# Performance work log

Hardware: AMD Instinct MI355X
Metric: run time of the kernel (lower is better)

The kernel has to match this reference:

```python
import jax, jax.numpy as jnp
import numpy as np

TOTAL_WORDS = 10000
EMB = 100
SEQ = 80
UNITS = 64
BATCH = 8192


def setup_inputs() -> dict:
    key = jax.random.key(0)
    ks = jax.random.split(key, 10)
    sc = 0.05
    return {
        "tokens": jax.random.randint(ks[0], (BATCH, SEQ), 0, TOTAL_WORDS, dtype=jnp.int32),
        "emb": jax.random.normal(ks[1], (TOTAL_WORDS, EMB), jnp.float32) * sc,
        "W1x": jax.random.normal(ks[2], (EMB, UNITS), jnp.float32) * sc,
        "W1h": jax.random.normal(ks[3], (UNITS, UNITS), jnp.float32) * sc,
        "b1": jnp.zeros((UNITS,), jnp.float32),
        "W2x": jax.random.normal(ks[4], (UNITS, UNITS), jnp.float32) * sc,
        "W2h": jax.random.normal(ks[5], (UNITS, UNITS), jnp.float32) * sc,
        "b2": jnp.zeros((UNITS,), jnp.float32),
        "Wd": jax.random.normal(ks[6], (UNITS, 1), jnp.float32) * sc,
        "bd": jnp.zeros((1,), jnp.float32),
    }


def _simple_rnn(x, Wx, Wh, b):
    # x: [B, T, D] -> all hidden states [B, T, H] (Keras SimpleRNN, tanh)
    B = x.shape[0]
    H = Wh.shape[0]
    h0 = jnp.zeros((B, H), x.dtype)

    def step(h, xt):
        h = jnp.tanh(xt @ Wx + h @ Wh + b)
        return h, h

    _, hs = jax.lax.scan(step, h0, jnp.swapaxes(x, 0, 1))  # hs: [T, B, H]
    return jnp.swapaxes(hs, 0, 1)


def reference(tokens, emb, W1x, W1h, b1, W2x, W2h, b2, Wd, bd):
    x = emb[tokens]                      # [B, T, EMB] embedding lookup
    h1 = _simple_rnn(x, W1x, W1h, b1)    # [B, T, U] return_sequences=True
    h2 = _simple_rnn(h1, W2x, W2h, b2)[:, -1, :]  # last state, [B, U]
    logits = h2 @ Wd + bd                # [B, 1]
    return jax.nn.sigmoid(logits)
```

## Files before the change

### kernel.cpp

```cpp
#include <hip/hip_runtime.h>
#include <hip/hip_bf16.h>

#define TOTALW 10000
#define BATCH 8192
#define SEQ   80
#define EMBD  100
#define UNITS 64
#define MB    16
#define NTHREADS 256
#define HPAD  80
#define TOKPAD 84

typedef __attribute__((ext_vector_type(8))) short short8;
typedef __attribute__((ext_vector_type(4))) float floatx4;

__device__ __forceinline__ short f2bf(float f) {
  unsigned u = __float_as_uint(f);
  u += 0x7FFFu + ((u >> 16) & 1u);
  return (short)(u >> 16);
}
__device__ __forceinline__ float bf2f(short s) {
  return __uint_as_float(((unsigned)(unsigned short)s) << 16);
}
__device__ __forceinline__ unsigned pkbf(float a, float b) {
#if __has_builtin(__builtin_amdgcn_cvt_pk_bf16_f32)
  typedef __attribute__((ext_vector_type(2))) __bf16 bf2_t;
  bf2_t v = __builtin_amdgcn_cvt_pk_bf16_f32(a, b);
  union { bf2_t v; unsigned u; } c; c.v = v;
  return c.u;
#else
  unsigned ua = __float_as_uint(a) + 0x8000u;
  unsigned ub = __float_as_uint(b) + 0x8000u;
#if __has_builtin(__builtin_amdgcn_perm)
  return __builtin_amdgcn_perm(ub, ua, 0x07060302u);
#else
  return (ub & 0xFFFF0000u) | (ua >> 16);
#endif
#endif
}
__device__ __forceinline__ float fast_tanh(float x) {
  const float t = x * x;
  float p = __builtin_fmaf(-0.0359280f, t, 0.1270784f);
  p = __builtin_fmaf(p, t, -0.3324617f);
  p = __builtin_fmaf(p, t, 0.9999660f);
  return x * p;
}
__device__ __forceinline__ unsigned pk2bf_rn(float a, float b) {
  __hip_bfloat162 h = __float22bfloat162_rn(float2{a, b});
  union { __hip_bfloat162 h2; unsigned u; } c; c.h2 = h;
  return c.u;
}

__launch_bounds__(256)
__global__ void emb_proj_mfma(const float* __restrict__ emb,
                              const float* __restrict__ W1x,
                              const float* __restrict__ b1,
                              float* __restrict__ xw) {
  __shared__ __align__(16) short Es[16][128];
  const int tid  = threadIdx.x;
  const int wave = tid >> 6;
  const int lane = tid & 63;
  const int li   = lane & 15;
  const int quad = lane >> 4;
  const int q4   = quad * 4;
  const int rowBase = blockIdx.x * 16;

  for (int task = tid; task < 16 * 25; task += 256) {
    const int r = task / 25, c = task % 25;
    const float4 v = *(const float4*)(emb + (rowBase + r) * EMBD + c * 4);
    *(int2*)(&Es[r][c * 4]) = make_int2((int)pk2bf_rn(v.x, v.y), (int)pk2bf_rn(v.z, v.w));
  }
  for (int task = tid; task < 224; task += 256) {
    const int r = task / 14, c = task % 14;
    *(int*)(&Es[r][100 + c * 2]) = 0;
  }
  short8 bw[4];
  #pragma unroll
  for (int kc = 0; kc < 4; ++kc) {
    short8 f;
    #pragma unroll
    for (int j = 0; j < 8; ++j) {
      const int k = kc * 32 + quad * 8 + j;
      f[j] = (k < EMBD) ? f2bf(W1x[k * UNITS + wave * 16 + li]) : (short)0;
    }
    bw[kc] = f;
  }
  const float bb = b1[wave * 16 + li];
  __syncthreads();

  floatx4 acc = {bb, bb, bb, bb};
  #pragma unroll
  for (int kc = 0; kc < 4; ++kc) {
    const short8 a = *(const short8*)(&Es[li][kc * 32 + quad * 8]);
    acc = __builtin_amdgcn_mfma_f32_16x16x32_bf16(a, bw[kc], acc, 0, 0, 0);
  }
  #pragma unroll
  for (int i = 0; i < 4; ++i)
    xw[(rowBase + q4 + i) * UNITS + wave * 16 + li] = acc[i];
}

__launch_bounds__(NTHREADS, 2)
__global__ void rnn2_kernel(const int* __restrict__ tokens,
                            const float* __restrict__ xw,
                            const float* __restrict__ W1h,
                            const float* __restrict__ W2x,
                            const float* __restrict__ W2h,
                            const float* __restrict__ b2,
                            const float* __restrict__ Wd,
                            const float* __restrict__ bd,
                            float* __restrict__ out)
{
  __shared__ __align__(16) short H1s[2][MB][HPAD];
  __shared__ __align__(16) short H2s[2][MB][HPAD];
  __shared__ __align__(16) int   tok[MB][TOKPAD];

  const int tid  = threadIdx.x;
  const int wave = tid >> 6;
  const int lane = tid & 63;
  const int li   = lane & 15;
  const int quad = lane >> 4;
  const int u     = wave * 16 + li;
  const int ubase = wave * 16 + quad * 4;
  const int rowBase = blockIdx.x * MB;

  for (int task = tid; task < MB * 20; task += NTHREADS) {
    const int r = task / 20, c = task % 20;
    *(int4*)(&tok[r][c * 4]) = *(const int4*)(tokens + (rowBase + r) * SEQ + c * 4);
  }
  for (int i = tid; i < MB * HPAD / 2; i += NTHREADS)
    ((int*)&H2s[1][0][0])[i] = 0;

  short8 w1h[2], w2x[2], w2h[2];
  #pragma unroll
  for (int kc = 0; kc < 2; ++kc) {
    short8 f, g, h;
    #pragma unroll
    for (int j = 0; j < 8; ++j) {
      const int k = kc * 32 + quad * 8 + j;
      f[j] = f2bf(W1h[k * UNITS + u]);
      g[j] = f2bf(W2x[k * UNITS + u]);
      h[j] = f2bf(W2h[k * UNITS + u]);
    }
    w1h[kc] = f; w2x[kc] = g; w2h[kc] = h;
  }
  const float4 b2f = *(const float4*)(b2 + ubase);

  __syncthreads();

  float4 xw_cur;
  {
    const int tk0 = tok[li][0];
    const float4 x0 = *(const float4*)(xw + tk0 * UNITS + ubase);
    const unsigned p0 = pkbf(fast_tanh(x0.x), fast_tanh(x0.y));
    const unsigned p1 = pkbf(fast_tanh(x0.z), fast_tanh(x0.w));
    *(int2*)(&H1s[0][li][ubase]) = make_int2((int)p0, (int)p1);
    const int tk1 = tok[li][1];
    xw_cur = *(const float4*)(xw + tk1 * UNITS + ubase);
  }
  int tkA = tok[li][2];
  int tkB = tok[li][3];
  __syncthreads();

#define STEP(T, CUR, NXT, TKU, PF)                                              \
  {                                                                             \
    float4 xwn;                                                                 \
    if (PF) {                                                                   \
      xwn = *(const float4*)(xw + (TKU) * UNITS + ubase);                       \
      const int tnx = ((T) + 4 < SEQ) ? (T) + 4 : SEQ - 1;                      \
      TKU = tok[li][tnx];                                                       \
    }                                                                           \
    const short8 h1a0 = *(const short8*)(&H1s[CUR][li][quad * 8]);              \
    const short8 h1a1 = *(const short8*)(&H1s[CUR][li][32 + quad * 8]);         \
    const short8 h2a0 = *(const short8*)(&H2s[NXT][li][quad * 8]);              \
    const short8 h2a1 = *(const short8*)(&H2s[NXT][li][32 + quad * 8]);         \
    floatx4 accA = {b2f.x, b2f.y, b2f.z, b2f.w};                                \
    floatx4 accB = {0.f, 0.f, 0.f, 0.f};                                        \
    accA = __builtin_amdgcn_mfma_f32_16x16x32_bf16(w2x[0], h1a0, accA, 0, 0, 0);\
    accB = __builtin_amdgcn_mfma_f32_16x16x32_bf16(w2h[0], h2a0, accB, 0, 0, 0);\
    accA = __builtin_amdgcn_mfma_f32_16x16x32_bf16(w2x[1], h1a1, accA, 0, 0, 0);\
    accB = __builtin_amdgcn_mfma_f32_16x16x32_bf16(w2h[1], h2a1, accB, 0, 0, 0);\
    floatx4 acc1 = {xw_cur.x, xw_cur.y, xw_cur.z, xw_cur.w};                    \
    acc1 = __builtin_amdgcn_mfma_f32_16x16x32_bf16(w1h[0], h1a0, acc1, 0, 0, 0);\
    acc1 = __builtin_amdgcn_mfma_f32_16x16x32_bf16(w1h[1], h1a1, acc1, 0, 0, 0);\
    const unsigned a0 = pkbf(fast_tanh(accA[0] + accB[0]),                      \
                             fast_tanh(accA[1] + accB[1]));                     \
    const unsigned a1 = pkbf(fast_tanh(accA[2] + accB[2]),                      \
                             fast_tanh(accA[3] + accB[3]));                     \
    *(int2*)(&H2s[CUR][li][ubase]) = make_int2((int)a0, (int)a1);               \
    const unsigned c0 = pkbf(fast_tanh(acc1[0]), fast_tanh(acc1[1]));           \
    const unsigned c1 = pkbf(fast_tanh(acc1[2]), fast_tanh(acc1[3]));           \
    *(int2*)(&H1s[NXT][li][ubase]) = make_int2((int)c0, (int)c1);               \
    if (PF) xw_cur = xwn;                                                       \
    __syncthreads();                                                            \
  }

  for (int t = 0; t < SEQ - 2; t += 2) {
    STEP(t, 0, 1, tkA, 1)
    STEP(t + 1, 1, 0, tkB, 1)
  }
  STEP(SEQ - 2, 0, 1, tkA, 0)

  {
    const short8 h1a0 = *(const short8*)(&H1s[1][li][quad * 8]);
    const short8 h1a1 = *(const short8*)(&H1s[1][li][32 + quad * 8]);
    const short8 h2a0 = *(const short8*)(&H2s[0][li][quad * 8]);
    const short8 h2a1 = *(const short8*)(&H2s[0][li][32 + quad * 8]);
    floatx4 accA = {b2f.x, b2f.y, b2f.z, b2f.w};
    floatx4 accB = {0.f, 0.f, 0.f, 0.f};
    accA = __builtin_amdgcn_mfma_f32_16x16x32_bf16(w2x[0], h1a0, accA, 0, 0, 0);
    accB = __builtin_amdgcn_mfma_f32_16x16x32_bf16(w2h[0], h2a0, accB, 0, 0, 0);
    accA = __builtin_amdgcn_mfma_f32_16x16x32_bf16(w2x[1], h1a1, accA, 0, 0, 0);
    accB = __builtin_amdgcn_mfma_f32_16x16x32_bf16(w2h[1], h2a1, accB, 0, 0, 0);
    const unsigned a0 = pkbf(fast_tanh(accA[0] + accB[0]),
                             fast_tanh(accA[1] + accB[1]));
    const unsigned a1 = pkbf(fast_tanh(accA[2] + accB[2]),
                             fast_tanh(accA[3] + accB[3]));
    *(int2*)(&H2s[1][li][ubase]) = make_int2((int)a0, (int)a1);
  }
  __syncthreads();

  if (tid < MB) {
    const short* hrow = &H2s[1][tid][0];
    float acc = bd[0];
    #pragma unroll
    for (int uu = 0; uu < UNITS; ++uu)
      acc += bf2f(hrow[uu]) * Wd[uu];
    out[rowBase + tid] = 1.0f / (1.0f + __expf(-acc));
  }
#undef STEP
}

extern "C" void kernel_launch(void* const* d_in, const int* in_sizes, int n_in,
                              void* d_out, int out_size, void* d_ws, size_t ws_size,
                              hipStream_t stream) {
  const int*   tokens = (const int*)d_in[0];
  const float* emb    = (const float*)d_in[1];
  const float* W1x    = (const float*)d_in[2];
  const float* W1h    = (const float*)d_in[3];
  const float* b1     = (const float*)d_in[4];
  const float* W2x    = (const float*)d_in[5];
  const float* W2h    = (const float*)d_in[6];
  const float* b2     = (const float*)d_in[7];
  const float* Wd     = (const float*)d_in[8];
  const float* bd     = (const float*)d_in[9];
  float* out = (float*)d_out;
  float* xw  = (float*)d_ws;

  emb_proj_mfma<<<TOTALW / 16, 256, 0, stream>>>(emb, W1x, b1, xw);
  rnn2_kernel<<<BATCH / MB, NTHREADS, 0, stream>>>(tokens, xw, W1h, W2x, W2h,
                                                   b2, Wd, bd, out);
}
```

Before: 109.1 us.

## Switch RNN to fp16 with packed half tanh, persistent projection grid, parallel head

Moves all MFMA operands and hidden-state storage from bf16 to fp16. The tanh polynomial is now evaluated on packed half2 vectors, with conversion done by a pkrtz cvt, which cuts VALU work in the serial recurrence step. The embedding projection kernel becomes a grid-stride loop over 512 blocks that loads its weights once per block. Other changes: the xw prefetch uses two alternating registers instead of a copy, the token tail is padded so the clamp disappears, and the final dense layer is split across 64 lanes with shuffle reductions. The risks are fp16 range and precision in the packed tanh polynomial and round-toward-zero conversion error.

```diff
diff --git a/kernel.cpp b/kernel.cpp
--- a/kernel.cpp
+++ b/kernel.cpp
@@ -11,44 +11,30 @@
 #define HPAD  80
 #define TOKPAD 84
 
-typedef __attribute__((ext_vector_type(8))) short short8;
+typedef __attribute__((ext_vector_type(8))) _Float16 half8;
+typedef __attribute__((ext_vector_type(2))) _Float16 half2v;
 typedef __attribute__((ext_vector_type(4))) float floatx4;
 
-__device__ __forceinline__ short f2bf(float f) {
-  unsigned u = __float_as_uint(f);
-  u += 0x7FFFu + ((u >> 16) & 1u);
-  return (short)(u >> 16);
-}
-__device__ __forceinline__ float bf2f(short s) {
-  return __uint_as_float(((unsigned)(unsigned short)s) << 16);
-}
-__device__ __forceinline__ unsigned pkbf(float a, float b) {
-#if __has_builtin(__builtin_amdgcn_cvt_pk_bf16_f32)
-  typedef __attribute__((ext_vector_type(2))) __bf16 bf2_t;
-  bf2_t v = __builtin_amdgcn_cvt_pk_bf16_f32(a, b);
-  union { bf2_t v; unsigned u; } c; c.v = v;
-  return c.u;
+__device__ __forceinline__ half2v pkh(float a, float b) {
+#if __has_builtin(__builtin_amdgcn_cvt_pkrtz)
+  return (half2v)__builtin_amdgcn_cvt_pkrtz(a, b);
 #else
-  unsigned ua = __float_as_uint(a) + 0x8000u;
-  unsigned ub = __float_as_uint(b) + 0x8000u;
-#if __has_builtin(__builtin_amdgcn_perm)
-  return __builtin_amdgcn_perm(ub, ua, 0x07060302u);
-#else
-  return (ub & 0xFFFF0000u) | (ua >> 16);
+  return half2v{(_Float16)a, (_Float16)b};
 #endif
-#endif
-}
-__device__ __forceinline__ float fast_tanh(float x) {
-  const float t = x * x;
-  float p = __builtin_fmaf(-0.0359280f, t, 0.1270784f);
-  p = __builtin_fmaf(p, t, -0.3324617f);
-  p = __builtin_fmaf(p, t, 0.9999660f);
+}
+__device__ __forceinline__ int h2i(half2v h) {
+  union { half2v h; int i; } c; c.h = h; return c.i;
+}
+__device__ __forceinline__ half2v pk_tanh(half2v x) {
+  const half2v c3 = {(_Float16)-0.0359280f, (_Float16)-0.0359280f};
+  const half2v c2 = {(_Float16) 0.1270784f, (_Float16) 0.1270784f};
+  const half2v c1 = {(_Float16)-0.3324617f, (_Float16)-0.3324617f};
+  const half2v c0 = {(_Float16) 0.9999660f, (_Float16) 0.9999660f};
+  const half2v t = x * x;
+  half2v p = __builtin_elementwise_fma(c3, t, c2);
+  p = __builtin_elementwise_fma(p, t, c1);
+  p = __builtin_elementwise_fma(p, t, c0);
   return x * p;
-}
-__device__ __forceinline__ unsigned pk2bf_rn(float a, float b) {
-  __hip_bfloat162 h = __float22bfloat162_rn(float2{a, b});
-  union { __hip_bfloat162 h2; unsigned u; } c; c.h2 = h;
-  return c.u;
 }
 
 __launch_bounds__(256)
@@ -56,47 +42,50 @@
                               const float* __restrict__ W1x,
                               const float* __restrict__ b1,
                               float* __restrict__ xw) {
-  __shared__ __align__(16) short Es[16][128];
+  __shared__ __align__(16) _Float16 Es[16][128];
   const int tid  = threadIdx.x;
   const int wave = tid >> 6;
   const int lane = tid & 63;
   const int li   = lane & 15;
   const int quad = lane >> 4;
   const int q4   = quad * 4;
-  const int rowBase = blockIdx.x * 16;
-
-  for (int task = tid; task < 16 * 25; task += 256) {
-    const int r = task / 25, c = task % 25;
-    const float4 v = *(const float4*)(emb + (rowBase + r) * EMBD + c * 4);
-    *(int2*)(&Es[r][c * 4]) = make_int2((int)pk2bf_rn(v.x, v.y), (int)pk2bf_rn(v.z, v.w));
-  }
-  for (int task = tid; task < 224; task += 256) {
+
+  half8 bw[4];
+  #pragma unroll
+  for (int kc = 0; kc < 4; ++kc) {
+    half8 f;
+    #pragma unroll
+    for (int j = 0; j < 8; ++j) {
+      const int k = kc * 32 + quad * 8 + j;
+      f[j] = (k < EMBD) ? (_Float16)W1x[k * UNITS + wave * 16 + li] : (_Float16)0.0f;
+    }
+    bw[kc] = f;
+  }
+  const float bb = b1[wave * 16 + li];
+
+  for (int task = tid; task < 16 * 14; task += 256) {
     const int r = task / 14, c = task % 14;
     *(int*)(&Es[r][100 + c * 2]) = 0;
   }
-  short8 bw[4];
-  #pragma unroll
-  for (int kc = 0; kc < 4; ++kc) {
-    short8 f;
-    #pragma unroll
-    for (int j = 0; j < 8; ++j) {
-      const int k = kc * 32 + quad * 8 + j;
-      f[j] = (k < EMBD) ? f2bf(W1x[k * UNITS + wave * 16 + li]) : (short)0;
-    }
-    bw[kc] = f;
-  }
-  const float bb = b1[wave * 16 + li];
-  __syncthreads();
-
-  floatx4 acc = {bb, bb, bb, bb};
-  #pragma unroll
-  for (int kc = 0; kc < 4; ++kc) {
-    const short8 a = *(const short8*)(&Es[li][kc * 32 + quad * 8]);
-    acc = __builtin_amdgcn_mfma_f32_16x16x32_bf16(a, bw[kc], acc, 0, 0, 0);
-  }
-  #pragma unroll
-  for (int i = 0; i < 4; ++i)
-    xw[(rowBase + q4 + i) * UNITS + wave * 16 + li] = acc[i];
+
+  for (int rowBase = blockIdx.x * 16; rowBase < TOTALW; rowBase += 512 * 16) {
+    __syncthreads();
+    for (int task = tid; task < 16 * 25; task += 256) {
+      const int r = task / 25, c = task % 25;
+      const float4 v = *(const float4*)(emb + (rowBase + r) * EMBD + c * 4);
+      *(int2*)(&Es[r][c * 4]) = make_int2(h2i(pkh(v.x, v.y)), h2i(pkh(v.z, v.w)));
+    }
+    __syncthreads();
+    floatx4 acc = {bb, bb, bb, bb};
+    #pragma unroll
+    for (int kc = 0; kc < 4; ++kc) {
+      const half8 a = *(const half8*)(&Es[li][kc * 32 + quad * 8]);
+      acc = __builtin_amdgcn_mfma_f32_16x16x32_f16(a, bw[kc], acc, 0, 0, 0);
+    }
+    #pragma unroll
+    for (int i = 0; i < 4; ++i)
+      xw[(rowBase + q4 + i) * UNITS + wave * 16 + li] = acc[i];
+  }
 }
 
 __launch_bounds__(NTHREADS, 2)
@@ -110,9 +99,9 @@
                             const float* __restrict__ bd,
                             float* __restrict__ out)
 {
-  __shared__ __align__(16) short H1s[2][MB][HPAD];
-  __shared__ __align__(16) short H2s[2][MB][HPAD];
-  __shared__ __align__(16) int   tok[MB][TOKPAD];
+  __shared__ __align__(16) _Float16 H1s[2][MB][HPAD];
+  __shared__ __align__(16) _Float16 H2s[2][MB][HPAD];
+  __shared__ __align__(16) int      tok[MB][TOKPAD];
 
   const int tid  = threadIdx.x;
   const int wave = tid >> 6;
@@ -127,105 +116,115 @@
     const int r = task / 20, c = task % 20;
     *(int4*)(&tok[r][c * 4]) = *(const int4*)(tokens + (rowBase + r) * SEQ + c * 4);
   }
+  for (int task = tid; task < MB * 4; task += NTHREADS)
+    tok[task >> 2][SEQ + (task & 3)] = 0;
   for (int i = tid; i < MB * HPAD / 2; i += NTHREADS)
     ((int*)&H2s[1][0][0])[i] = 0;
 
-  short8 w1h[2], w2x[2], w2h[2];
+  half8 w1h[2], w2x[2], w2h[2];
   #pragma unroll
   for (int kc = 0; kc < 2; ++kc) {
-    short8 f, g, h;
+    half8 f, g, h;
     #pragma unroll
     for (int j = 0; j < 8; ++j) {
       const int k = kc * 32 + quad * 8 + j;
-      f[j] = f2bf(W1h[k * UNITS + u]);
-      g[j] = f2bf(W2x[k * UNITS + u]);
-      h[j] = f2bf(W2h[k * UNITS + u]);
+      f[j] = (_Float16)W1h[k * UNITS + u];
+      g[j] = (_Float16)W2x[k * UNITS + u];
+      h[j] = (_Float16)W2h[k * UNITS + u];
     }
     w1h[kc] = f; w2x[kc] = g; w2h[kc] = h;
   }
   const float4 b2f = *(const float4*)(b2 + ubase);
 
+  float4 wdv[4];
+  float  bdv = 0.f;
+  if (wave == 0) {
+    const int s = lane & 3;
+    #pragma unroll
+    for (int i = 0; i < 4; ++i)
+      wdv[i] = *(const float4*)(Wd + s * 16 + i * 4);
+    bdv = bd[0];
+  }
+
   __syncthreads();
 
-  float4 xw_cur;
+  float4 xw0, xw1;
   {
     const int tk0 = tok[li][0];
     const float4 x0 = *(const float4*)(xw + tk0 * UNITS + ubase);
-    const unsigned p0 = pkbf(fast_tanh(x0.x), fast_tanh(x0.y));
-    const unsigned p1 = pkbf(fast_tanh(x0.z), fast_tanh(x0.w));
-    *(int2*)(&H1s[0][li][ubase]) = make_int2((int)p0, (int)p1);
+    *(int2*)(&H1s[0][li][ubase]) = make_int2(h2i(pk_tanh(pkh(x0.x, x0.y))),
+                                             h2i(pk_tanh(pkh(x0.z, x0.w))));
     const int tk1 = tok[li][1];
-    xw_cur = *(const float4*)(xw + tk1 * UNITS + ubase);
+    xw0 = *(const float4*)(xw + tk1 * UNITS + ubase);
   }
   int tkA = tok[li][2];
   int tkB = tok[li][3];
   __syncthreads();
 
-#define STEP(T, CUR, NXT, TKU, PF)                                              \
+#define STEP(T, CUR, NXT, TKU, PF, XWC, XWN)                                    \
   {                                                                             \
-    float4 xwn;                                                                 \
     if (PF) {                                                                   \
-      xwn = *(const float4*)(xw + (TKU) * UNITS + ubase);                       \
-      const int tnx = ((T) + 4 < SEQ) ? (T) + 4 : SEQ - 1;                      \
-      TKU = tok[li][tnx];                                                       \
+      XWN = *(const float4*)(xw + (TKU) * UNITS + ubase);                       \
+      TKU = tok[li][(T) + 4];                                                   \
     }                                                                           \
-    const short8 h1a0 = *(const short8*)(&H1s[CUR][li][quad * 8]);              \
-    const short8 h1a1 = *(const short8*)(&H1s[CUR][li][32 + quad * 8]);         \
-    const short8 h2a0 = *(const short8*)(&H2s[NXT][li][quad * 8]);              \
-    const short8 h2a1 = *(const short8*)(&H2s[NXT][li][32 + quad * 8]);         \
+    const half8 h1a0 = *(const half8*)(&H1s[CUR][li][quad * 8]);                \
+    const half8 h1a1 = *(const half8*)(&H1s[CUR][li][32 + quad * 8]);           \
+    const half8 h2a0 = *(const half8*)(&H2s[NXT][li][quad * 8]);                \
+    const half8 h2a1 = *(const half8*)(&H2s[NXT][li][32 + quad * 8]);           \
     floatx4 accA = {b2f.x, b2f.y, b2f.z, b2f.w};                                \
     floatx4 accB = {0.f, 0.f, 0.f, 0.f};                                        \
-    accA = __builtin_amdgcn_mfma_f32_16x16x32_bf16(w2x[0], h1a0, accA, 0, 0, 0);\
-    accB = __builtin_amdgcn_mfma_f32_16x16x32_bf16(w2h[0], h2a0, accB, 0, 0, 0);\
-    accA = __builtin_amdgcn_mfma_f32_16x16x32_bf16(w2x[1], h1a1, accA, 0, 0, 0);\
-    accB = __builtin_amdgcn_mfma_f32_16x16x32_bf16(w2h[1], h2a1, accB, 0, 0, 0);\
-    floatx4 acc1 = {xw_cur.x, xw_cur.y, xw_cur.z, xw_cur.w};                    \
-    acc1 = __builtin_amdgcn_mfma_f32_16x16x32_bf16(w1h[0], h1a0, acc1, 0, 0, 0);\
-    acc1 = __builtin_amdgcn_mfma_f32_16x16x32_bf16(w1h[1], h1a1, acc1, 0, 0, 0);\
-    const unsigned a0 = pkbf(fast_tanh(accA[0] + accB[0]),                      \
-                             fast_tanh(accA[1] + accB[1]));                     \
-    const unsigned a1 = pkbf(fast_tanh(accA[2] + accB[2]),                      \
-                             fast_tanh(accA[3] + accB[3]));                     \
-    *(int2*)(&H2s[CUR][li][ubase]) = make_int2((int)a0, (int)a1);               \
-    const unsigned c0 = pkbf(fast_tanh(acc1[0]), fast_tanh(acc1[1]));           \
-    const unsigned c1 = pkbf(fast_tanh(acc1[2]), fast_tanh(acc1[3]));           \
-    *(int2*)(&H1s[NXT][li][ubase]) = make_int2((int)c0, (int)c1);               \
-    if (PF) xw_cur = xwn;                                                       \
+    accA = __builtin_amdgcn_mfma_f32_16x16x32_f16(w2x[0], h1a0, accA, 0, 0, 0); \
+    accB = __builtin_amdgcn_mfma_f32_16x16x32_f16(w2h[0], h2a0, accB, 0, 0, 0); \
+    accA = __builtin_amdgcn_mfma_f32_16x16x32_f16(w2x[1], h1a1, accA, 0, 0, 0); \
+    accB = __builtin_amdgcn_mfma_f32_16x16x32_f16(w2h[1], h2a1, accB, 0, 0, 0); \
+    floatx4 acc1 = {(XWC).x, (XWC).y, (XWC).z, (XWC).w};                        \
+    acc1 = __builtin_amdgcn_mfma_f32_16x16x32_f16(w1h[0], h1a0, acc1, 0, 0, 0); \
+    acc1 = __builtin_amdgcn_mfma_f32_16x16x32_f16(w1h[1], h1a1, acc1, 0, 0, 0); \
+    const half2v s0 = pk_tanh(pkh(accA[0] + accB[0], accA[1] + accB[1]));       \
+    const half2v s1 = pk_tanh(pkh(accA[2] + accB[2], accA[3] + accB[3]));       \
+    *(int2*)(&H2s[CUR][li][ubase]) = make_int2(h2i(s0), h2i(s1));               \
+    const half2v c0 = pk_tanh(pkh(acc1[0], acc1[1]));                           \
+    const half2v c1 = pk_tanh(pkh(acc1[2], acc1[3]));                           \
+    *(int2*)(&H1s[NXT][li][ubase]) = make_int2(h2i(c0), h2i(c1));               \
     __syncthreads();                                                            \
   }
 
   for (int t = 0; t < SEQ - 2; t += 2) {
-    STEP(t, 0, 1, tkA, 1)
-    STEP(t + 1, 1, 0, tkB, 1)
-  }
-  STEP(SEQ - 2, 0, 1, tkA, 0)
+    STEP(t,     0, 1, tkA, 1, xw0, xw1)
+    STEP(t + 1, 1, 0, tkB, 1, xw1, xw0)
+  }
+  STEP(SEQ - 2, 0, 1, tkA, 0, xw0, xw1)
 
   {
-    const short8 h1a0 = *(const short8*)(&H1s[1][li][quad * 8]);
-    const short8 h1a1 = *(const short8*)(&H1s[1][li][32 + quad * 8]);
-    const short8 h2a0 = *(const short8*)(&H2s[0][li][quad * 8]);
-    const short8 h2a1 = *(const short8*)(&H2s[0][li][32 + quad * 8]);
+    const half8 h1a0 = *(const half8*)(&H1s[1][li][quad * 8]);
+    const half8 h1a1 = *(const half8*)(&H1s[1][li][32 + quad * 8]);
+    const half8 h2a0 = *(const half8*)(&H2s[0][li][quad * 8]);
+    const half8 h2a1 = *(const half8*)(&H2s[0][li][32 + quad * 8]);
     floatx4 accA = {b2f.x, b2f.y, b2f.z, b2f.w};
     floatx4 accB = {0.f, 0.f, 0.f, 0.f};
-    accA = __builtin_amdgcn_mfma_f32_16x16x32_bf16(w2x[0], h1a0, accA, 0, 0, 0);
-    accB = __builtin_amdgcn_mfma_f32_16x16x32_bf16(w2h[0], h2a0, accB, 0, 0, 0);
-    accA = __builtin_amdgcn_mfma_f32_16x16x32_bf16(w2x[1], h1a1, accA, 0, 0, 0);
-    accB = __builtin_amdgcn_mfma_f32_16x16x32_bf16(w2h[1], h2a1, accB, 0, 0, 0);
-    const unsigned a0 = pkbf(fast_tanh(accA[0] + accB[0]),
-                             fast_tanh(accA[1] + accB[1]));
-    const unsigned a1 = pkbf(fast_tanh(accA[2] + accB[2]),
-                             fast_tanh(accA[3] + accB[3]));
-    *(int2*)(&H2s[1][li][ubase]) = make_int2((int)a0, (int)a1);
+    accA = __builtin_amdgcn_mfma_f32_16x16x32_f16(w2x[0], h1a0, accA, 0, 0, 0);
+    accB = __builtin_amdgcn_mfma_f32_16x16x32_f16(w2h[0], h2a0, accB, 0, 0, 0);
+    accA = __builtin_amdgcn_mfma_f32_16x16x32_f16(w2x[1], h1a1, accA, 0, 0, 0);
+    accB = __builtin_amdgcn_mfma_f32_16x16x32_f16(w2h[1], h2a1, accB, 0, 0, 0);
+    const half2v s0 = pk_tanh(pkh(accA[0] + accB[0], accA[1] + accB[1]));
+    const half2v s1 = pk_tanh(pkh(accA[2] + accB[2], accA[3] + accB[3]));
+    *(int2*)(&H2s[1][li][ubase]) = make_int2(h2i(s0), h2i(s1));
   }
   __syncthreads();
 
-  if (tid < MB) {
-    const short* hrow = &H2s[1][tid][0];
-    float acc = bd[0];
-    #pragma unroll
-    for (int uu = 0; uu < UNITS; ++uu)
-      acc += bf2f(hrow[uu]) * Wd[uu];
-    out[rowBase + tid] = 1.0f / (1.0f + __expf(-acc));
+  if (wave == 0) {
+    const int r = lane >> 2, s = lane & 3;
+    const _Float16* hrow = &H2s[1][r][0];
+    float acc = 0.f;
+    #pragma unroll
+    for (int i = 0; i < 4; ++i) {
+      const int base = s * 16 + i * 4;
+      acc += (float)hrow[base + 0] * wdv[i].x + (float)hrow[base + 1] * wdv[i].y
+           + (float)hrow[base + 2] * wdv[i].z + (float)hrow[base + 3] * wdv[i].w;
+    }
+    acc += __shfl_xor(acc, 1);
+    acc += __shfl_xor(acc, 2);
+    if (s == 0) out[rowBase + r] = 1.0f / (1.0f + __expf(-(acc + bdv)));
   }
 #undef STEP
 }
@@ -246,7 +245,7 @@
   float* out = (float*)d_out;
   float* xw  = (float*)d_ws;
 
-  emb_proj_mfma<<<TOTALW / 16, 256, 0, stream>>>(emb, W1x, b1, xw);
+  emb_proj_mfma<<<512, 256, 0, stream>>>(emb, W1x, b1, xw);
   rnn2_kernel<<<BATCH / MB, NTHREADS, 0, stream>>>(tokens, xw, W1h, W2x, W2h,
                                                    b2, Wd, bd, out);
 }
```

After: 106.6 us. -2.3%, faster.
